# Kernel tuning notes

Measured on AMD Instinct MI355X. Metric: run time of the kernel, lower is better.

## Reference

```python
import jax, jax.numpy as jnp
import numpy as np

N = 100000
DIM = 128
N_EDGES = 3200000
EPS = 1e-5


def setup_inputs() -> dict:
    key = jax.random.key(0)
    k1, k2, k3, k4, k5, k6 = jax.random.split(key, 6)
    x = jax.random.normal(k1, (N, DIM), dtype=jnp.float32)
    edge_row = jnp.sort(jax.random.randint(k2, (N_EDGES,), 0, N, dtype=jnp.int64))
    edge_col = jax.random.randint(k3, (N_EDGES,), 0, N, dtype=jnp.int64)
    edge_val = jax.random.uniform(k4, (N_EDGES,), dtype=jnp.float32)
    gamma = jnp.ones((DIM,), dtype=jnp.float32)
    beta = jnp.zeros((DIM,), dtype=jnp.float32)
    return {"x": x, "edge_row": edge_row, "edge_col": edge_col,
            "edge_val": edge_val, "gamma": gamma, "beta": beta}


def _layernorm(h, gamma, beta):
    mu = jnp.mean(h, axis=-1, keepdims=True)
    var = jnp.mean(jnp.square(h - mu), axis=-1, keepdims=True)
    return (h - mu) * jax.lax.rsqrt(var + EPS) * gamma + beta


def reference(x, edge_row, edge_col, edge_val, gamma, beta):
    # sparse adj @ x  ==  segment-sum of val * x[src] into dst rows
    msgs = edge_val[:, None] * x[edge_col]            # [E, DIM]
    h = jax.ops.segment_sum(msgs, edge_row, num_segments=N)  # [N, DIM]
    return _layernorm(h + x, gamma, beta)
```

## Files before the change

### kernel.cpp

```cpp
#include <hip/hip_runtime.h>
#include <hip/hip_fp16.h>

#define DIM 128
#define EPS 1e-5f
#define WPB 4
#define UF  4

typedef float vfloat2 __attribute__((ext_vector_type(2)));

__global__ void prep_kernel(const float4* __restrict__ x4,
                            __half2* __restrict__ xh2,
                            const int* __restrict__ edge_row,
                            int* __restrict__ row_ptr,
                            int n4, int n_nodes, int n_edges)
{
    int i = blockIdx.x * blockDim.x + threadIdx.x;
    if (i < n4) {
        float4 v = x4[i];
        xh2[2 * i]     = __float22half2_rn(make_float2(v.x, v.y));
        xh2[2 * i + 1] = __float22half2_rn(make_float2(v.z, v.w));
    }
    if (i < n_edges) {
        int cur  = edge_row[i];
        int prev = (i == 0) ? -1 : edge_row[i - 1];
        for (int r = prev + 1; r <= cur; ++r) row_ptr[r] = i;
        if (i == n_edges - 1) {
            for (int r = cur + 1; r <= n_nodes; ++r) row_ptr[r] = n_edges;
        }
    }
}

__global__ __launch_bounds__(WPB * 64)
void gnn_fused_kernel(const uint4* __restrict__ xh16,
                      const int*   __restrict__ row_ptr,
                      const int*   __restrict__ edge_col,
                      const float* __restrict__ edge_val,
                      const float* __restrict__ gamma,
                      const float* __restrict__ beta,
                      float*       __restrict__ out,
                      int n_nodes, int n_edges)
{
    const int wave = threadIdx.x >> 6;
    const int lane = threadIdx.x & 63;
    const int q    = lane >> 4;
    const int sub  = lane & 15;
    const int node = blockIdx.x * WPB + wave;
    if (node >= n_nodes) return;

    const int start = row_ptr[node];
    const int end   = row_ptr[node + 1];
    const unsigned len = (unsigned)(end - start);

    float acc[8];
#pragma unroll
    for (int k = 0; k < 8; ++k) acc[k] = 0.f;

    const int ebase = start & ~3;
    const int emax  = n_edges - 4;
    for (int e0 = ebase; e0 < end; e0 += 4 * UF) {
        const int b  = e0 + 4 * q;
        const int bc = min(b, emax);
        int4   c4 = *(const int4*)  (edge_col + bc);
        float4 w4 = *(const float4*)(edge_val + bc);

        int   c[UF] = {c4.x, c4.y, c4.z, c4.w};
        float w[UF] = {w4.x, w4.y, w4.z, w4.w};

        const int off = b - start;
#pragma unroll
        for (int u = 0; u < UF; ++u) {
            bool in = (unsigned)(off + u) < len;
            c[u] = in ? c[u] : 0;
            w[u] = in ? w[u] : 0.f;
        }

        uint4 v[UF];
#pragma unroll
        for (int u = 0; u < UF; ++u)
            v[u] = xh16[c[u] * (DIM / 8) + sub];

#pragma unroll
        for (int u = 0; u < UF; ++u) {
            const __half* hp = (const __half*)&v[u];
#pragma unroll
            for (int j = 0; j < 8; ++j)
                acc[j] = fmaf(w[u], __half2float(hp[j]), acc[j]);
        }
    }

#pragma unroll
    for (int k = 0; k < 8; ++k) {
        acc[k] += __shfl_xor(acc[k], 16, 64);
        acc[k] += __shfl_xor(acc[k], 32, 64);
    }

    uint4 xv = xh16[node * (DIM / 8) + sub];
    const __half* xp = (const __half*)&xv;
    float h[8];
#pragma unroll
    for (int j = 0; j < 8; ++j) h[j] = acc[j] + __half2float(xp[j]);

    float s = 0.f, sq = 0.f;
#pragma unroll
    for (int k = 0; k < 8; ++k) { s += h[k]; sq += h[k] * h[k]; }
#pragma unroll
    for (int off = 1; off <= 8; off <<= 1) {
        s  += __shfl_xor(s,  off, 64);
        sq += __shfl_xor(sq, off, 64);
    }
    const float mean = s * (1.0f / (float)DIM);
    const float var  = sq * (1.0f / (float)DIM) - mean * mean;
    const float rs   = rsqrtf(var + EPS);

    float hx = (q < 2) ? ((q == 0) ? h[0] : h[2]) : ((q == 2) ? h[4] : h[6]);
    float hy = (q < 2) ? ((q == 0) ? h[1] : h[3]) : ((q == 2) ? h[5] : h[7]);
    const int didx = sub * 4 + q;
    const float2 g = ((const float2*)gamma)[didx];
    const float2 b = ((const float2*)beta)[didx];
    vfloat2 o;
    o.x = (hx - mean) * rs * g.x + b.x;
    o.y = (hy - mean) * rs * g.y + b.y;
    __builtin_nontemporal_store(o, (vfloat2*)out + node * (DIM / 2) + didx);
}

extern "C" void kernel_launch(void* const* d_in, const int* in_sizes, int n_in,
                              void* d_out, int out_size, void* d_ws, size_t ws_size,
                              hipStream_t stream)
{
    const float* x        = (const float*)d_in[0];
    const int*   edge_row = (const int*)  d_in[1];
    const int*   edge_col = (const int*)  d_in[2];
    const float* edge_val = (const float*)d_in[3];
    const float* gamma    = (const float*)d_in[4];
    const float* beta     = (const float*)d_in[5];
    float*       out      = (float*)d_out;

    const int n_nodes = in_sizes[0] / DIM;
    const int n_edges = in_sizes[1];
    const int n_elem  = in_sizes[0];
    const int n4      = n_elem / 4;

    __half2* xh2     = (__half2*)d_ws;
    int*     row_ptr = (int*)((char*)d_ws + (size_t)n_elem * sizeof(__half));

    int prep_threads = (n4 > n_edges) ? n4 : n_edges;
    prep_kernel<<<(prep_threads + 255) / 256, 256, 0, stream>>>(
        (const float4*)x, xh2, edge_row, row_ptr, n4, n_nodes, n_edges);

    const int blocks = (n_nodes + WPB - 1) / WPB;
    gnn_fused_kernel<<<blocks, WPB * 64, 0, stream>>>(
        (const uint4*)d_ws, row_ptr, edge_col, edge_val, gamma, beta, out,
        n_nodes, n_edges);
}
```

Measured before the change: 235.4 us.

## Process two nodes per wave with 8-edge lanes and unmasked steady-state loop

Each 64-lane wave now handles two nodes (32 lanes each), with each half-wave split into two groups that each gather 8 edges per trip instead of four groups of 4. The edge loop is split into a masked head, an unmasked steady-state body and a masked tail, so bounds checks drop out of the main loop. The cross-group reduction needs one fewer shuffle, and output stores widen to float4. Lane utilisation should improve on low-degree rows (about 32 edges on average). The cost is more registers per lane for 8 in-flight gathers and fewer gather groups per node.

```diff
diff --git a/kernel.cpp b/kernel.cpp
--- a/kernel.cpp
+++ b/kernel.cpp
@@ -3,10 +3,10 @@
 
 #define DIM 128
 #define EPS 1e-5f
-#define WPB 4
-#define UF  4
+#define WPB 8
+#define EPT 16
 
-typedef float vfloat2 __attribute__((ext_vector_type(2)));
+typedef float vfloat4 __attribute__((ext_vector_type(4)));
 
 __global__ void prep_kernel(const float4* __restrict__ x4,
                             __half2* __restrict__ xh2,
@@ -30,6 +30,47 @@
     }
 }
 
+template<bool MASKED>
+__device__ __forceinline__
+void edge_trip(int e0, int q, int sub, int start, unsigned len, int emax,
+               const uint4* __restrict__ xh16,
+               const int*   __restrict__ edge_col,
+               const float* __restrict__ edge_val,
+               float acc[8])
+{
+    const int b = e0 + 8 * q;
+    int b0 = b, b1 = b + 4;
+    if (MASKED) { b0 = min(b0, emax); b1 = min(b1, emax); }
+
+    int4   c4a = *(const int4*)  (edge_col + b0);
+    int4   c4b = *(const int4*)  (edge_col + b1);
+    float4 w4a = *(const float4*)(edge_val + b0);
+    float4 w4b = *(const float4*)(edge_val + b1);
+
+    int   c[8] = {c4a.x, c4a.y, c4a.z, c4a.w, c4b.x, c4b.y, c4b.z, c4b.w};
+    float w[8] = {w4a.x, w4a.y, w4a.z, w4a.w, w4b.x, w4b.y, w4b.z, w4b.w};
+
+    if (MASKED) {
+        const int off = b - start;
+#pragma unroll
+        for (int u = 0; u < 8; ++u)
+            w[u] = ((unsigned)(off + u) < len) ? w[u] : 0.f;
+    }
+
+    uint4 v[8];
+#pragma unroll
+    for (int u = 0; u < 8; ++u)
+        v[u] = xh16[c[u] * (DIM / 8) + sub];
+
+#pragma unroll
+    for (int u = 0; u < 8; ++u) {
+        const __half* hp = (const __half*)&v[u];
+#pragma unroll
+        for (int j = 0; j < 8; ++j)
+            acc[j] = fmaf(w[u], __half2float(hp[j]), acc[j]);
+    }
+}
+
 __global__ __launch_bounds__(WPB * 64)
 void gnn_fused_kernel(const uint4* __restrict__ xh16,
                       const int*   __restrict__ row_ptr,
@@ -42,59 +83,43 @@
 {
     const int wave = threadIdx.x >> 6;
     const int lane = threadIdx.x & 63;
-    const int q    = lane >> 4;
+    const int q    = (lane >> 4) & 1;
     const int sub  = lane & 15;
-    const int node = blockIdx.x * WPB + wave;
+    const int node = (blockIdx.x * WPB + wave) * 2 + (lane >> 5);
     if (node >= n_nodes) return;
 
     const int start = row_ptr[node];
     const int end   = row_ptr[node + 1];
     const unsigned len = (unsigned)(end - start);
 
+    const uint4 xv = xh16[node * (DIM / 8) + sub];
+
     float acc[8];
 #pragma unroll
     for (int k = 0; k < 8; ++k) acc[k] = 0.f;
 
+    const int emax  = n_edges - 4;
     const int ebase = start & ~3;
-    const int emax  = n_edges - 4;
-    for (int e0 = ebase; e0 < end; e0 += 4 * UF) {
-        const int b  = e0 + 4 * q;
-        const int bc = min(b, emax);
-        int4   c4 = *(const int4*)  (edge_col + bc);
-        float4 w4 = *(const float4*)(edge_val + bc);
-
-        int   c[UF] = {c4.x, c4.y, c4.z, c4.w};
-        float w[UF] = {w4.x, w4.y, w4.z, w4.w};
-
-        const int off = b - start;
-#pragma unroll
-        for (int u = 0; u < UF; ++u) {
-            bool in = (unsigned)(off + u) < len;
-            c[u] = in ? c[u] : 0;
-            w[u] = in ? w[u] : 0.f;
-        }
-
-        uint4 v[UF];
-#pragma unroll
-        for (int u = 0; u < UF; ++u)
-            v[u] = xh16[c[u] * (DIM / 8) + sub];
-
-#pragma unroll
-        for (int u = 0; u < UF; ++u) {
-            const __half* hp = (const __half*)&v[u];
-#pragma unroll
-            for (int j = 0; j < 8; ++j)
-                acc[j] = fmaf(w[u], __half2float(hp[j]), acc[j]);
-        }
+    int e0 = ebase;
+    if (e0 < end) {
+        edge_trip<true>(e0, q, sub, start, len, emax,
+                        xh16, edge_col, edge_val, acc);
+        e0 += EPT;
+    }
+    while (e0 + EPT <= end) {
+        edge_trip<false>(e0, q, sub, start, len, emax,
+                         xh16, edge_col, edge_val, acc);
+        e0 += EPT;
+    }
+    if (e0 < end) {
+        edge_trip<true>(e0, q, sub, start, len, emax,
+                        xh16, edge_col, edge_val, acc);
     }
 
 #pragma unroll
-    for (int k = 0; k < 8; ++k) {
+    for (int k = 0; k < 8; ++k)
         acc[k] += __shfl_xor(acc[k], 16, 64);
-        acc[k] += __shfl_xor(acc[k], 32, 64);
-    }
 
-    uint4 xv = xh16[node * (DIM / 8) + sub];
     const __half* xp = (const __half*)&xv;
     float h[8];
 #pragma unroll
@@ -112,15 +137,19 @@
     const float var  = sq * (1.0f / (float)DIM) - mean * mean;
     const float rs   = rsqrtf(var + EPS);
 
-    float hx = (q < 2) ? ((q == 0) ? h[0] : h[2]) : ((q == 2) ? h[4] : h[6]);
-    float hy = (q < 2) ? ((q == 0) ? h[1] : h[3]) : ((q == 2) ? h[5] : h[7]);
-    const int didx = sub * 4 + q;
-    const float2 g = ((const float2*)gamma)[didx];
-    const float2 b = ((const float2*)beta)[didx];
-    vfloat2 o;
-    o.x = (hx - mean) * rs * g.x + b.x;
-    o.y = (hy - mean) * rs * g.y + b.y;
-    __builtin_nontemporal_store(o, (vfloat2*)out + node * (DIM / 2) + didx);
+    float h0 = q ? h[4] : h[0];
+    float h1 = q ? h[5] : h[1];
+    float h2 = q ? h[6] : h[2];
+    float h3 = q ? h[7] : h[3];
+    const int didx = sub * 2 + q;
+    const float4 gm = ((const float4*)gamma)[didx];
+    const float4 bt = ((const float4*)beta)[didx];
+    vfloat4 o;
+    o.x = (h0 - mean) * rs * gm.x + bt.x;
+    o.y = (h1 - mean) * rs * gm.y + bt.y;
+    o.z = (h2 - mean) * rs * gm.z + bt.z;
+    o.w = (h3 - mean) * rs * gm.w + bt.w;
+    __builtin_nontemporal_store(o, (vfloat4*)out + node * (DIM / 4) + didx);
 }
 
 extern "C" void kernel_launch(void* const* d_in, const int* in_sizes, int n_in,
@@ -147,7 +176,8 @@
     prep_kernel<<<(prep_threads + 255) / 256, 256, 0, stream>>>(
         (const float4*)x, xh2, edge_row, row_ptr, n4, n_nodes, n_edges);
 
-    const int blocks = (n_nodes + WPB - 1) / WPB;
+    const int nodes_per_block = WPB * 2;
+    const int blocks = (n_nodes + nodes_per_block - 1) / nodes_per_block;
     gnn_fused_kernel<<<blocks, WPB * 64, 0, stream>>>(
         (const uint4*)d_ws, row_ptr, edge_col, edge_val, gamma, beta, out,
         n_nodes, n_edges);
```

After: 250.6 us. 1.06x slower.

## Software-pipeline edge gathers with double-buffered index and feature loads

Applied to the files above, without the earlier changes.

Restructures the per-node edge loop into a two-stage software pipeline. Index and weight loads run one tile ahead and feature gathers for the next tile are issued before the FMAs of the current tile, so the latency of the dependent index-then-gather chain overlaps with compute. The self-feature load is hoisted to the kernel start for the same reason. In exchange it uses more registers for the double buffers, which may lower occupancy, and it adds extra prefetch loads past the end of each row.

```diff
diff --git a/kernel.cpp b/kernel.cpp
--- a/kernel.cpp
+++ b/kernel.cpp
@@ -4,7 +4,7 @@
 #define DIM 128
 #define EPS 1e-5f
 #define WPB 4
-#define UF  4
+#define EPT 16
 
 typedef float vfloat2 __attribute__((ext_vector_type(2)));
 
@@ -27,6 +27,41 @@
         if (i == n_edges - 1) {
             for (int r = cur + 1; r <= n_nodes; ++r) row_ptr[r] = n_edges;
         }
+    }
+}
+
+__device__ __forceinline__
+void mask_edges(int4 rc, float4 rw, int off, unsigned len,
+                int c[4], float w[4])
+{
+    const int   cc[4] = {rc.x, rc.y, rc.z, rc.w};
+    const float ww[4] = {rw.x, rw.y, rw.z, rw.w};
+#pragma unroll
+    for (int u = 0; u < 4; ++u) {
+        const bool in = (unsigned)(off + u) < len;
+        c[u] = in ? cc[u] : 0;
+        w[u] = in ? ww[u] : 0.f;
+    }
+}
+
+__device__ __forceinline__
+void issue_gathers(const uint4* __restrict__ xh16, const int c[4], int sub,
+                   uint4 v[4])
+{
+#pragma unroll
+    for (int u = 0; u < 4; ++u)
+        v[u] = xh16[c[u] * (DIM / 8) + sub];
+}
+
+__device__ __forceinline__
+void do_fma(const uint4 v[4], const float w[4], float acc[8])
+{
+#pragma unroll
+    for (int u = 0; u < 4; ++u) {
+        const __half* hp = (const __half*)&v[u];
+#pragma unroll
+        for (int j = 0; j < 8; ++j)
+            acc[j] = fmaf(w[u], __half2float(hp[j]), acc[j]);
     }
 }
 
@@ -51,40 +86,54 @@
     const int end   = row_ptr[node + 1];
     const unsigned len = (unsigned)(end - start);
 
+    const uint4 xv = xh16[node * (DIM / 8) + sub];
+
     float acc[8];
 #pragma unroll
     for (int k = 0; k < 8; ++k) acc[k] = 0.f;
 
     const int ebase = start & ~3;
+    const int T     = (end > ebase) ? ((end - ebase + 15) >> 4) : 0;
     const int emax  = n_edges - 4;
-    for (int e0 = ebase; e0 < end; e0 += 4 * UF) {
-        const int b  = e0 + 4 * q;
-        const int bc = min(b, emax);
-        int4   c4 = *(const int4*)  (edge_col + bc);
-        float4 w4 = *(const float4*)(edge_val + bc);
-
-        int   c[UF] = {c4.x, c4.y, c4.z, c4.w};
-        float w[UF] = {w4.x, w4.y, w4.z, w4.w};
-
-        const int off = b - start;
-#pragma unroll
-        for (int u = 0; u < UF; ++u) {
-            bool in = (unsigned)(off + u) < len;
-            c[u] = in ? c[u] : 0;
-            w[u] = in ? w[u] : 0.f;
+
+    if (T > 0) {
+        int c[4];
+        float wA[4], wB[4];
+        uint4 vA[4], vB[4];
+
+        int bA = ebase + 4 * q;
+        {
+            const int bc = min(bA, emax);
+            int4   rc = *(const int4*)  (edge_col + bc);
+            float4 rw = *(const float4*)(edge_val + bc);
+            mask_edges(rc, rw, bA - start, len, c, wA);
         }
-
-        uint4 v[UF];
-#pragma unroll
-        for (int u = 0; u < UF; ++u)
-            v[u] = xh16[c[u] * (DIM / 8) + sub];
-
-#pragma unroll
-        for (int u = 0; u < UF; ++u) {
-            const __half* hp = (const __half*)&v[u];
-#pragma unroll
-            for (int j = 0; j < 8; ++j)
-                acc[j] = fmaf(w[u], __half2float(hp[j]), acc[j]);
+        int bB = bA + EPT;
+        int4   rcB = *(const int4*)  (edge_col + min(bB, emax));
+        float4 rwB = *(const float4*)(edge_val + min(bB, emax));
+        issue_gathers(xh16, c, sub, vA);
+
+        int4 rcA; float4 rwA;
+        int t = 0;
+        for (;;) {
+            if (t + 1 >= T) { do_fma(vA, wA, acc); break; }
+            mask_edges(rcB, rwB, bB - start, len, c, wB);
+            const int b2 = bB + EPT;
+            rcA = *(const int4*)  (edge_col + min(b2, emax));
+            rwA = *(const float4*)(edge_val + min(b2, emax));
+            issue_gathers(xh16, c, sub, vB);
+            do_fma(vA, wA, acc);
+
+            if (t + 2 >= T) { do_fma(vB, wB, acc); break; }
+            mask_edges(rcA, rwA, b2 - start, len, c, wA);
+            const int b3 = b2 + EPT;
+            rcB = *(const int4*)  (edge_col + min(b3, emax));
+            rwB = *(const float4*)(edge_val + min(b3, emax));
+            issue_gathers(xh16, c, sub, vA);
+            do_fma(vB, wB, acc);
+
+            t += 2;
+            bB = b3;
         }
     }
 
@@ -94,7 +143,6 @@
         acc[k] += __shfl_xor(acc[k], 32, 64);
     }
 
-    uint4 xv = xh16[node * (DIM / 8) + sub];
     const __half* xp = (const __half*)&xv;
     float h[8];
 #pragma unroll
```

Measured after the change: 261.3 us. +11.0%, slower.
